# Kernel tuning notes

Measured on AMD Instinct MI355X. Metric: run time of the kernel, lower is better.

The kernel has to match this reference:

```python
import jax, jax.numpy as jnp
import numpy as np

B, D_IN, H, D_OUT, E = 16384, 512, 1024, 512, 4


def setup_inputs() -> dict:
    key = jax.random.key(0)
    ks = jax.random.split(key, 8)
    x = jax.random.normal(ks[0], (B, D_IN), dtype=jnp.float32)
    command = jax.random.randint(ks[1], (B,), 0, E, dtype=jnp.int64)
    # Per-branch Encoder params: Linear(D_IN->H), Linear(H->H), Linear(H->D_OUT)
    s = 0.02
    W1 = jax.random.normal(ks[2], (E, D_IN, H), dtype=jnp.float32) * s
    b1 = jnp.zeros((E, H), dtype=jnp.float32)
    W2 = jax.random.normal(ks[3], (E, H, H), dtype=jnp.float32) * s
    b2 = jnp.zeros((E, H), dtype=jnp.float32)
    W3 = jax.random.normal(ks[4], (E, H, D_OUT), dtype=jnp.float32) * s
    b3 = jnp.zeros((E, D_OUT), dtype=jnp.float32)
    return {"x": x, "command": command, "W1": W1, "b1": b1,
            "W2": W2, "b2": b2, "W3": W3, "b3": b3}


def reference(x, command, W1, b1, W2, b2, W3, b3):
    # Evaluate all branches as batched GEMMs, then select per-sample branch.
    # Mathematically identical to per-sample dispatch in the torch module.
    h = jax.nn.relu(jnp.einsum('bi,eih->beh', x, W1) + b1)        # [B,E,H]
    h = jax.nn.relu(jnp.einsum('beh,ehk->bek', h, W2) + b2)       # [B,E,H]
    y = jnp.tanh(jnp.einsum('bek,eko->beo', h, W3) + b3)          # [B,E,D_OUT]
    # select branch output per sample according to command
    idx = command.astype(jnp.int32)[:, None, None]                # [B,1,1]
    out = jnp.take_along_axis(y, idx, axis=1)[:, 0, :]            # [B,D_OUT]
    return out
```

## Files before the change

kernel.cpp:

```cpp
#include <hip/hip_runtime.h>


#define B_N   16384
#define E_N   4
#define DIN   512
#define HID   1024
#define DOUT  512

typedef __attribute__((ext_vector_type(8))) short bf16x8;
typedef __attribute__((ext_vector_type(4))) float f32x4;
typedef __attribute__((address_space(3))) unsigned int lds_u32;
typedef const __attribute__((address_space(1))) unsigned int glb_u32;

__device__ __forceinline__ void gll16(const void* g, void* l) {
    __builtin_amdgcn_global_load_lds((glb_u32*)g, (lds_u32*)l, 16, 0, 0);
}

__device__ __forceinline__ unsigned short f2bf(float f) {
    unsigned int u = __float_as_uint(f);
    u += 0x7FFFu + ((u >> 16) & 1u);
    return (unsigned short)(u >> 16);
}

__device__ __forceinline__ float fast_tanh(float x) {
    x = fminf(fmaxf(x, -9.0f), 9.0f);
    float t = __builtin_amdgcn_exp2f(x * 2.8853900817779268f);
    return (t - 1.0f) * __builtin_amdgcn_rcpf(t + 1.0f);
}

__global__ void zero_ctrl_k(int* ctrl) {
    if (threadIdx.x < 16) ctrl[threadIdx.x] = 0;
}

__global__ void count_k(const int* __restrict__ cmd, int* __restrict__ ctrl) {
    int i = blockIdx.x * 256 + threadIdx.x;
    int e = cmd[i] & 3;
    int lane = threadIdx.x & 63;
#pragma unroll
    for (int ee = 0; ee < 4; ++ee) {
        unsigned long long mask = __ballot(e == ee);
        int leader = __ffsll((unsigned long long)mask) - 1;
        if (mask && lane == leader)
            atomicAdd(&ctrl[ee], __popcll(mask));
    }
}

__global__ void plan_k(int* __restrict__ ctrl, int* __restrict__ tileExpert,
                       int* __restrict__ tileBase) {
    if (threadIdx.x == 0) {
        int P = 0, nt = 0;
        for (int e = 0; e < 4; ++e) {
            ctrl[8 + e] = P;
            int c = ctrl[e];
            int tiles = (c + 127) >> 7;
            for (int t = 0; t < tiles; ++t) {
                tileExpert[nt] = e;
                tileBase[nt] = P + t * 128;
                ++nt;
            }
            P += tiles * 128;
        }
        ctrl[12] = P;
        ctrl[13] = nt;
    }
}

__global__ void scatter_k(const int* __restrict__ cmd, int* __restrict__ ctrl,
                          int* __restrict__ perm) {
    int i = blockIdx.x * 256 + threadIdx.x;
    int e = cmd[i] & 3;
    int lane = threadIdx.x & 63;
#pragma unroll
    for (int ee = 0; ee < 4; ++ee) {
        unsigned long long mask = __ballot(e == ee);
        if (e == ee) {
            int leader = __ffsll((unsigned long long)mask) - 1;
            int rank = __popcll(mask & ((1ull << lane) - 1ull));
            int wbase = 0;
            if (lane == leader)
                wbase = atomicAdd(&ctrl[4 + ee], __popcll(mask));
            wbase = __builtin_amdgcn_readfirstlane(wbase);
            perm[ctrl[8 + ee] + wbase + rank] = i;
        }
    }
}

__global__ void fillpad_k(const int* __restrict__ ctrl, int* __restrict__ perm) {
    for (int e = 0; e < 4; ++e) {
        int c = ctrl[e];
        int base = ctrl[8 + e];
        int padded = ctrl[8 + e + 1] - base;
        for (int j = c + (int)threadIdx.x; j < padded; j += (int)blockDim.x)
            perm[base + j] = perm[base];
    }
}

template<int KD, int ND>
__global__ __launch_bounds__(256) void transw_k(const float* __restrict__ W,
                                                unsigned short* __restrict__ Wt) {
    __shared__ float t[32][33];
    int e = blockIdx.z;
    size_t base = (size_t)e * KD * ND;
    int k0 = blockIdx.x * 32, n0 = blockIdx.y * 32;
    int tx = threadIdx.x & 31, ty = threadIdx.x >> 5;
#pragma unroll
    for (int s = 0; s < 4; ++s)
        t[ty + s * 8][tx] = W[base + (size_t)(k0 + ty + s * 8) * ND + n0 + tx];
    __syncthreads();
#pragma unroll
    for (int s = 0; s < 4; ++s)
        Wt[base + (size_t)(n0 + ty + s * 8) * KD + k0 + tx] = f2bf(t[tx][ty + s * 8]);
}

template<int K, int N, int ACT, bool GATHER_A, bool SCATTER_OUT>
__global__ __launch_bounds__(256) void gemm_k(
    const void* __restrict__ Asrc, const unsigned short* __restrict__ Bt,
    const float* __restrict__ bias, void* __restrict__ Outp,
    const int* __restrict__ ctrl, const int* __restrict__ tileExpert,
    const int* __restrict__ tileBase, const int* __restrict__ perm)
{
    const int nTiles = ctrl[13];
    if ((int)blockIdx.x >= nTiles) return;
    const int e = tileExpert[blockIdx.x];
    const int rowBase = tileBase[blockIdx.x];
    const int n0 = blockIdx.y * 128;

    constexpr int AST = GATHER_A ? 40 : 32;
    __shared__ unsigned short Als[128][AST];
    __shared__ unsigned short Bls[128][32];

    const int tid = threadIdx.x;
    const int lane = tid & 63;
    const int w = tid >> 6;
    const int wm = w >> 1, wn = w & 1;
    const int lr = lane & 15, lh = lane >> 4;

    f32x4 acc[4][4] = {};

    const int sr = tid >> 2;
    const int sc = (tid & 3) * 8;
    const unsigned short* Bb = Bt + ((size_t)e * N + (size_t)n0) * K;
    const unsigned short* Ab = (const unsigned short*)Asrc + (size_t)rowBase * K;

    const float* Af = (const float*)Asrc;
    int arow[4];
    if (GATHER_A) {
#pragma unroll
        for (int s = 0; s < 4; ++s)
            arow[s] = perm[rowBase + s * 32 + (tid >> 3)];
    }

    for (int kb = 0; kb < K / 32; ++kb) {
        const int k0 = kb * 32;
        float4 areg[4];
        if (GATHER_A) {
#pragma unroll
            for (int s = 0; s < 4; ++s)
                areg[s] = *(const float4*)(Af + (size_t)arow[s] * K + k0 + (tid & 7) * 4);
        }
        __syncthreads();
        gll16(Bb + (size_t)sr * K + k0 + sc, &Bls[sr][sc]);
        gll16(Bb + (size_t)(sr + 64) * K + k0 + sc, &Bls[sr + 64][sc]);
        if (GATHER_A) {
#pragma unroll
            for (int s = 0; s < 4; ++s) {
                int row = s * 32 + (tid >> 3);
                ushort4 packed = make_ushort4(f2bf(areg[s].x), f2bf(areg[s].y),
                                              f2bf(areg[s].z), f2bf(areg[s].w));
                *(ushort4*)&Als[row][(tid & 7) * 4] = packed;
            }
        } else {
            gll16(Ab + (size_t)sr * K + k0 + sc, &Als[sr][sc]);
            gll16(Ab + (size_t)(sr + 64) * K + k0 + sc, &Als[sr + 64][sc]);
        }
        __syncthreads();
        bf16x8 afr[4], bfr[4];
#pragma unroll
        for (int mi = 0; mi < 4; ++mi)
            afr[mi] = *(const bf16x8*)&Als[wm * 64 + mi * 16 + lr][lh * 8];
#pragma unroll
        for (int ni = 0; ni < 4; ++ni)
            bfr[ni] = *(const bf16x8*)&Bls[wn * 64 + ni * 16 + lr][lh * 8];
#pragma unroll
        for (int mi = 0; mi < 4; ++mi)
#pragma unroll
            for (int ni = 0; ni < 4; ++ni)
                acc[mi][ni] = __builtin_amdgcn_mfma_f32_16x16x32_bf16(
                    afr[mi], bfr[ni], acc[mi][ni], 0, 0, 0);
    }

    float bv[4];
    int colv[4];
#pragma unroll
    for (int ni = 0; ni < 4; ++ni) {
        colv[ni] = n0 + wn * 64 + ni * 16 + lr;
        bv[ni] = bias[e * N + colv[ni]];
    }
#pragma unroll
    for (int mi = 0; mi < 4; ++mi) {
#pragma unroll
        for (int r = 0; r < 4; ++r) {
            int rowL = wm * 64 + mi * 16 + lh * 4 + r;
            int gRow = rowBase + rowL;
            int orow = SCATTER_OUT ? perm[gRow] : gRow;
#pragma unroll
            for (int ni = 0; ni < 4; ++ni) {
                float v = acc[mi][ni][r] + bv[ni];
                if (ACT == 0) v = fmaxf(v, 0.0f);
                else          v = fast_tanh(v);
                if (SCATTER_OUT)
                    ((float*)Outp)[(size_t)orow * N + colv[ni]] = v;
                else
                    ((unsigned short*)Outp)[(size_t)orow * N + colv[ni]] = f2bf(v);
            }
        }
    }
}

extern "C" void kernel_launch(void* const* d_in, const int* in_sizes, int n_in,
                              void* d_out, int out_size, void* d_ws, size_t ws_size,
                              hipStream_t stream) {
    const float* x  = (const float*)d_in[0];
    const int*   cmd= (const int*)d_in[1];
    const float* W1 = (const float*)d_in[2];
    const float* b1 = (const float*)d_in[3];
    const float* W2 = (const float*)d_in[4];
    const float* b2 = (const float*)d_in[5];
    const float* W3 = (const float*)d_in[6];
    const float* b3 = (const float*)d_in[7];
    float* out = (float*)d_out;

    char* w = (char*)d_ws;
    int* ctrl       = (int*)w;
    int* tileExpert = ctrl + 64;
    int* tileBase   = ctrl + 224;
    int* perm       = ctrl + 512;
    unsigned short* Wt1 = (unsigned short*)(w + (1u << 17));
    unsigned short* Wt2 = (unsigned short*)(w + (1u << 17) + (4u << 20));
    unsigned short* Wt3 = (unsigned short*)(w + (1u << 17) + (12u << 20));
    unsigned short* h1  = (unsigned short*)(w + (1u << 17) + (16u << 20));
    unsigned short* h2  = h1 + (size_t)16896 * 1024;

    zero_ctrl_k<<<1, 64, 0, stream>>>(ctrl);
    count_k<<<B_N / 256, 256, 0, stream>>>(cmd, ctrl);
    plan_k<<<1, 64, 0, stream>>>(ctrl, tileExpert, tileBase);
    scatter_k<<<B_N / 256, 256, 0, stream>>>(cmd, ctrl, perm);
    fillpad_k<<<1, 256, 0, stream>>>(ctrl, perm);

    transw_k<512, 1024><<<dim3(16, 32, 4), 256, 0, stream>>>(W1, Wt1);
    transw_k<1024, 1024><<<dim3(32, 32, 4), 256, 0, stream>>>(W2, Wt2);
    transw_k<1024, 512><<<dim3(32, 16, 4), 256, 0, stream>>>(W3, Wt3);

    gemm_k<512, 1024, 0, true, false><<<dim3(136, 8), 256, 0, stream>>>(
        x, Wt1, b1, h1, ctrl, tileExpert, tileBase, perm);
    gemm_k<1024, 1024, 0, false, false><<<dim3(136, 8), 256, 0, stream>>>(
        h1, Wt2, b2, h2, ctrl, tileExpert, tileBase, perm);
    gemm_k<1024, 512, 1, false, true><<<dim3(136, 4), 256, 0, stream>>>(
        h2, Wt3, b3, out, ctrl, tileExpert, tileBase, perm);
}
```

Measured before the change: 183.1 us.

## Merge routing and prep kernels, pre-gather x to bf16, widen GEMM tiles

Combines the count, zero and plan kernels into one single-block kernel. The three weight transposes, the padding fill and a new gather-and-convert of x into a permuted bf16 buffer are merged into one prep launch. GEMM1 can then use the same direct-to-LDS load path as the other layers. The GEMM moves to 512-thread blocks with 128x256 output tiles, halving the N-grid to reuse A tiles more. This cuts launch count and per-tile gather cost, but adds an extra pass over x and a larger LDS footprint per block.

```diff
diff --git a/kernel.cpp b/kernel.cpp
--- a/kernel.cpp
+++ b/kernel.cpp
@@ -2,10 +2,10 @@
 
 
 #define B_N   16384
-#define E_N   4
 #define DIN   512
 #define HID   1024
 #define DOUT  512
+#define MAXTILES 136
 
 typedef __attribute__((ext_vector_type(8))) short bf16x8;
 typedef __attribute__((ext_vector_type(4))) float f32x4;
@@ -28,31 +28,27 @@
     return (t - 1.0f) * __builtin_amdgcn_rcpf(t + 1.0f);
 }
 
-__global__ void zero_ctrl_k(int* ctrl) {
-    if (threadIdx.x < 16) ctrl[threadIdx.x] = 0;
-}
-
-__global__ void count_k(const int* __restrict__ cmd, int* __restrict__ ctrl) {
-    int i = blockIdx.x * 256 + threadIdx.x;
-    int e = cmd[i] & 3;
-    int lane = threadIdx.x & 63;
-#pragma unroll
-    for (int ee = 0; ee < 4; ++ee) {
-        unsigned long long mask = __ballot(e == ee);
-        int leader = __ffsll((unsigned long long)mask) - 1;
-        if (mask && lane == leader)
-            atomicAdd(&ctrl[ee], __popcll(mask));
-    }
-}
-
-__global__ void plan_k(int* __restrict__ ctrl, int* __restrict__ tileExpert,
-                       int* __restrict__ tileBase) {
-    if (threadIdx.x == 0) {
+__global__ void plan_all_k(const int* __restrict__ cmd, int* __restrict__ ctrl,
+                           int* __restrict__ tileExpert, int* __restrict__ tileBase) {
+    __shared__ int h[4];
+    int tid = threadIdx.x;
+    if (tid < 4) h[tid] = 0;
+    __syncthreads();
+    int c0 = 0, c1 = 0, c2 = 0, c3 = 0;
+    for (int i = tid; i < B_N; i += 256) {
+        int e = cmd[i] & 3;
+        c0 += (e == 0); c1 += (e == 1); c2 += (e == 2); c3 += (e == 3);
+    }
+    atomicAdd(&h[0], c0); atomicAdd(&h[1], c1);
+    atomicAdd(&h[2], c2); atomicAdd(&h[3], c3);
+    __syncthreads();
+    if (tid == 0) {
         int P = 0, nt = 0;
         for (int e = 0; e < 4; ++e) {
+            ctrl[e] = h[e];
+            ctrl[4 + e] = 0;
             ctrl[8 + e] = P;
-            int c = ctrl[e];
-            int tiles = (c + 127) >> 7;
+            int tiles = (h[e] + 127) >> 7;
             for (int t = 0; t < tiles; ++t) {
                 tileExpert[nt] = e;
                 tileBase[nt] = P + t * 128;
@@ -85,102 +81,99 @@
     }
 }
 
-__global__ void fillpad_k(const int* __restrict__ ctrl, int* __restrict__ perm) {
-    for (int e = 0; e < 4; ++e) {
-        int c = ctrl[e];
-        int base = ctrl[8 + e];
-        int padded = ctrl[8 + e + 1] - base;
-        for (int j = c + (int)threadIdx.x; j < padded; j += (int)blockDim.x)
-            perm[base + j] = perm[base];
-    }
-}
-
-template<int KD, int ND>
-__global__ __launch_bounds__(256) void transw_k(const float* __restrict__ W,
-                                                unsigned short* __restrict__ Wt) {
-    __shared__ float t[32][33];
-    int e = blockIdx.z;
-    size_t base = (size_t)e * KD * ND;
-    int k0 = blockIdx.x * 32, n0 = blockIdx.y * 32;
-    int tx = threadIdx.x & 31, ty = threadIdx.x >> 5;
-#pragma unroll
-    for (int s = 0; s < 4; ++s)
-        t[ty + s * 8][tx] = W[base + (size_t)(k0 + ty + s * 8) * ND + n0 + tx];
-    __syncthreads();
-#pragma unroll
-    for (int s = 0; s < 4; ++s)
-        Wt[base + (size_t)(n0 + ty + s * 8) * KD + k0 + tx] = f2bf(t[tx][ty + s * 8]);
-}
-
-template<int K, int N, int ACT, bool GATHER_A, bool SCATTER_OUT>
-__global__ __launch_bounds__(256) void gemm_k(
-    const void* __restrict__ Asrc, const unsigned short* __restrict__ Bt,
+__global__ __launch_bounds__(256) void prep_data_k(
+    const float* __restrict__ W1, const float* __restrict__ W2,
+    const float* __restrict__ W3, unsigned short* __restrict__ Wt1,
+    unsigned short* __restrict__ Wt2, unsigned short* __restrict__ Wt3,
+    const float* __restrict__ x, unsigned short* __restrict__ xp,
+    int* __restrict__ perm, const int* __restrict__ ctrl)
+{
+    int b = blockIdx.x;
+    if (b < 8192) {
+        int e = b >> 11, r = b & 2047;
+        const float* W; unsigned short* Wt; int KD, ND, kt, nt;
+        if (r < 512)       { W = W1; Wt = Wt1; KD = 512;  ND = 1024; kt = r & 15;           nt = r >> 4; }
+        else if (r < 1536) { W = W2; Wt = Wt2; KD = 1024; ND = 1024; kt = (r - 512) & 31;   nt = (r - 512) >> 5; }
+        else               { W = W3; Wt = Wt3; KD = 1024; ND = 512;  kt = (r - 1536) & 31;  nt = (r - 1536) >> 5; }
+        __shared__ float t[32][33];
+        size_t base = (size_t)e * KD * ND;
+        int k0 = kt * 32, n0 = nt * 32;
+        int tx = threadIdx.x & 31, ty = threadIdx.x >> 5;
+#pragma unroll
+        for (int s = 0; s < 4; ++s)
+            t[ty + s * 8][tx] = W[base + (size_t)(k0 + ty + s * 8) * ND + n0 + tx];
+        __syncthreads();
+#pragma unroll
+        for (int s = 0; s < 4; ++s)
+            Wt[base + (size_t)(n0 + ty + s * 8) * KD + k0 + tx] = f2bf(t[tx][ty + s * 8]);
+    } else {
+        int g = b - 8192;
+        int p = g * 4 + (int)(threadIdx.x >> 6);
+        if (p >= ctrl[12]) return;
+        int lane = threadIdx.x & 63;
+        int e = (p >= ctrl[9]) + (p >= ctrl[10]) + (p >= ctrl[11]);
+        int segBase = ctrl[8 + e];
+        int src;
+        if (p < segBase + ctrl[e]) {
+            src = perm[p];
+        } else {
+            src = perm[segBase];
+            if (lane == 0) perm[p] = src;
+        }
+        const float* xr = x + (size_t)src * DIN + lane * 8;
+        float4 a = *(const float4*)xr;
+        float4 c = *(const float4*)(xr + 4);
+        uint4 o;
+        o.x = (unsigned)f2bf(a.x) | ((unsigned)f2bf(a.y) << 16);
+        o.y = (unsigned)f2bf(a.z) | ((unsigned)f2bf(a.w) << 16);
+        o.z = (unsigned)f2bf(c.x) | ((unsigned)f2bf(c.y) << 16);
+        o.w = (unsigned)f2bf(c.z) | ((unsigned)f2bf(c.w) << 16);
+        *(uint4*)(xp + (size_t)p * DIN + lane * 8) = o;
+    }
+}
+
+template<int K, int N, int ACT, bool SCATTER_OUT>
+__global__ __launch_bounds__(512) void gemm_k(
+    const unsigned short* __restrict__ A, const unsigned short* __restrict__ Bt,
     const float* __restrict__ bias, void* __restrict__ Outp,
     const int* __restrict__ ctrl, const int* __restrict__ tileExpert,
     const int* __restrict__ tileBase, const int* __restrict__ perm)
 {
-    const int nTiles = ctrl[13];
-    if ((int)blockIdx.x >= nTiles) return;
+    if ((int)blockIdx.x >= ctrl[13]) return;
     const int e = tileExpert[blockIdx.x];
     const int rowBase = tileBase[blockIdx.x];
-    const int n0 = blockIdx.y * 128;
-
-    constexpr int AST = GATHER_A ? 40 : 32;
-    __shared__ unsigned short Als[128][AST];
-    __shared__ unsigned short Bls[128][32];
+    const int n0 = blockIdx.y * 256;
+
+    __shared__ unsigned short Als[128 * 32];
+    __shared__ unsigned short Bls[256 * 32];
 
     const int tid = threadIdx.x;
     const int lane = tid & 63;
     const int w = tid >> 6;
-    const int wm = w >> 1, wn = w & 1;
+    const int wm = w >> 2, wn = w & 3;
     const int lr = lane & 15, lh = lane >> 4;
 
     f32x4 acc[4][4] = {};
 
     const int sr = tid >> 2;
     const int sc = (tid & 3) * 8;
-    const unsigned short* Bb = Bt + ((size_t)e * N + (size_t)n0) * K;
-    const unsigned short* Ab = (const unsigned short*)Asrc + (size_t)rowBase * K;
-
-    const float* Af = (const float*)Asrc;
-    int arow[4];
-    if (GATHER_A) {
-#pragma unroll
-        for (int s = 0; s < 4; ++s)
-            arow[s] = perm[rowBase + s * 32 + (tid >> 3)];
-    }
+    const unsigned short* Ab = A + (size_t)rowBase * K;
+    const unsigned short* Bb = Bt + ((size_t)e * N + n0) * K;
 
     for (int kb = 0; kb < K / 32; ++kb) {
         const int k0 = kb * 32;
-        float4 areg[4];
-        if (GATHER_A) {
-#pragma unroll
-            for (int s = 0; s < 4; ++s)
-                areg[s] = *(const float4*)(Af + (size_t)arow[s] * K + k0 + (tid & 7) * 4);
-        }
         __syncthreads();
-        gll16(Bb + (size_t)sr * K + k0 + sc, &Bls[sr][sc]);
-        gll16(Bb + (size_t)(sr + 64) * K + k0 + sc, &Bls[sr + 64][sc]);
-        if (GATHER_A) {
-#pragma unroll
-            for (int s = 0; s < 4; ++s) {
-                int row = s * 32 + (tid >> 3);
-                ushort4 packed = make_ushort4(f2bf(areg[s].x), f2bf(areg[s].y),
-                                              f2bf(areg[s].z), f2bf(areg[s].w));
-                *(ushort4*)&Als[row][(tid & 7) * 4] = packed;
-            }
-        } else {
-            gll16(Ab + (size_t)sr * K + k0 + sc, &Als[sr][sc]);
-            gll16(Ab + (size_t)(sr + 64) * K + k0 + sc, &Als[sr + 64][sc]);
-        }
+        gll16(Ab + (size_t)sr * K + k0 + sc, &Als[sr * 32 + sc]);
+        gll16(Bb + (size_t)sr * K + k0 + sc, &Bls[sr * 32 + sc]);
+        gll16(Bb + (size_t)(sr + 128) * K + k0 + sc, &Bls[(sr + 128) * 32 + sc]);
         __syncthreads();
         bf16x8 afr[4], bfr[4];
 #pragma unroll
         for (int mi = 0; mi < 4; ++mi)
-            afr[mi] = *(const bf16x8*)&Als[wm * 64 + mi * 16 + lr][lh * 8];
+            afr[mi] = *(const bf16x8*)&Als[(wm * 64 + mi * 16 + lr) * 32 + lh * 8];
 #pragma unroll
         for (int ni = 0; ni < 4; ++ni)
-            bfr[ni] = *(const bf16x8*)&Bls[wn * 64 + ni * 16 + lr][lh * 8];
+            bfr[ni] = *(const bf16x8*)&Bls[(wn * 64 + ni * 16 + lr) * 32 + lh * 8];
 #pragma unroll
         for (int mi = 0; mi < 4; ++mi)
 #pragma unroll
@@ -235,26 +228,22 @@
     int* tileExpert = ctrl + 64;
     int* tileBase   = ctrl + 224;
     int* perm       = ctrl + 512;
-    unsigned short* Wt1 = (unsigned short*)(w + (1u << 17));
-    unsigned short* Wt2 = (unsigned short*)(w + (1u << 17) + (4u << 20));
-    unsigned short* Wt3 = (unsigned short*)(w + (1u << 17) + (12u << 20));
-    unsigned short* h1  = (unsigned short*)(w + (1u << 17) + (16u << 20));
-    unsigned short* h2  = h1 + (size_t)16896 * 1024;
-
-    zero_ctrl_k<<<1, 64, 0, stream>>>(ctrl);
-    count_k<<<B_N / 256, 256, 0, stream>>>(cmd, ctrl);
-    plan_k<<<1, 64, 0, stream>>>(ctrl, tileExpert, tileBase);
+    unsigned short* Wt1 = (unsigned short*)(w + 131072);
+    unsigned short* Wt2 = (unsigned short*)(w + 131072 + 4194304);
+    unsigned short* Wt3 = (unsigned short*)(w + 131072 + 12582912);
+    unsigned short* h1  = (unsigned short*)(w + 131072 + 16777216);
+    unsigned short* h2  = h1 + (size_t)16896 * HID;
+    unsigned short* xp  = h2;
+
+    plan_all_k<<<1, 256, 0, stream>>>(cmd, ctrl, tileExpert, tileBase);
     scatter_k<<<B_N / 256, 256, 0, stream>>>(cmd, ctrl, perm);
-    fillpad_k<<<1, 256, 0, stream>>>(ctrl, perm);
-
-    transw_k<512, 1024><<<dim3(16, 32, 4), 256, 0, stream>>>(W1, Wt1);
-    transw_k<1024, 1024><<<dim3(32, 32, 4), 256, 0, stream>>>(W2, Wt2);
-    transw_k<1024, 512><<<dim3(32, 16, 4), 256, 0, stream>>>(W3, Wt3);
-
-    gemm_k<512, 1024, 0, true, false><<<dim3(136, 8), 256, 0, stream>>>(
-        x, Wt1, b1, h1, ctrl, tileExpert, tileBase, perm);
-    gemm_k<1024, 1024, 0, false, false><<<dim3(136, 8), 256, 0, stream>>>(
+    prep_data_k<<<8192 + 4224, 256, 0, stream>>>(W1, W2, W3, Wt1, Wt2, Wt3,
+                                                 x, xp, perm, ctrl);
+
+    gemm_k<DIN, HID, 0, false><<<dim3(MAXTILES, 4), 512, 0, stream>>>(
+        xp, Wt1, b1, h1, ctrl, tileExpert, tileBase, perm);
+    gemm_k<HID, HID, 0, false><<<dim3(MAXTILES, 4), 512, 0, stream>>>(
         h1, Wt2, b2, h2, ctrl, tileExpert, tileBase, perm);
-    gemm_k<1024, 512, 1, false, true><<<dim3(136, 4), 256, 0, stream>>>(
+    gemm_k<HID, DOUT, 1, true><<<dim3(MAXTILES, 2), 512, 0, stream>>>(
         h2, Wt3, b3, out, ctrl, tileExpert, tileBase, perm);
 }
```

Measured after the change: 195.1 us. +6.5%, slower.
